# Optimization experiments

Measured on AMD Instinct MI355X. Metric: run time of the kernel, lower is better.

The kernel has to match this reference:

```python
import jax, jax.numpy as jnp
from jax import lax
import numpy as np

NEG = -10000.0

def sequence_mask(length, max_len):
    # [B, max_len] bool
    return jnp.arange(max_len)[None, :] < length[:, None]

def mdn_loss(logp, text_lengths, mel_lengths):
    # logp: [B, T_seq, T_mel]; CTC-style forward recursion over T_mel
    B, T_seq, T_mel = logp.shape
    init = jnp.full((B, T_seq), NEG, logp.dtype).at[:, 0].set(logp[:, 0, 0])
    logp_t = jnp.moveaxis(logp, 2, 0)  # [T_mel, B, T_seq]

    def step(alpha, lp):  # alpha: [B, T_seq]
        shifted = jnp.concatenate(
            [jnp.full((B, 1), NEG, alpha.dtype), alpha[:, :-1]], axis=1)
        new = jnp.logaddexp(alpha + 1e-4, shifted + 1e-4) + lp
        return new, new

    _, cols = lax.scan(step, init, logp_t[1:])
    log_alpha = jnp.concatenate([init[None], cols], axis=0)  # [T_mel, B, T_seq]
    alpha_last = log_alpha[mel_lengths - 1, jnp.arange(B), text_lengths - 1]
    return -alpha_last.mean() / T_seq

def mse_loss_masked(x, target, length):
    # seq_len_norm=False branch: sum of masked squared error / mask.sum() over expanded mask
    B, T, D = x.shape
    mask = sequence_mask(length, T)[:, :, None].astype(x.dtype)  # [B, T, 1]
    diff = x * mask - target * mask
    return jnp.sum(diff * diff) / (jnp.sum(mask) * D)

def sample_wise_min_max(x, mask):
    # x: [B, T, D], mask: [B, T, 1] bool; min/max over dims (1,2)
    maximum = jnp.max(jnp.where(mask, x, 0.0), axis=(1, 2), keepdims=True)
    minimum = jnp.min(jnp.where(mask, x, jnp.inf), axis=(1, 2), keepdims=True)
    return (x - minimum) / (maximum - minimum + 1e-8)

def _gaussian_kernel(size=11, sigma=1.5):
    coords = jnp.arange(size, dtype=jnp.float32) - (size - 1) / 2.0
    g = jnp.exp(-(coords ** 2) / (2.0 * sigma ** 2))
    g = g / g.sum()
    return jnp.outer(g, g)

def _ssim_mean(x, y):
    # x, y: [B, 1, H, W]; 11x11 gaussian SSIM, VALID conv, k1=0.01, k2=0.03, data_range=1
    k = _gaussian_kernel()[None, None].astype(x.dtype)  # [1,1,11,11]
    conv = lambda z: lax.conv_general_dilated(z, k, (1, 1), 'VALID')
    mu_x, mu_y = conv(x), conv(y)
    sxx = conv(x * x) - mu_x * mu_x
    syy = conv(y * y) - mu_y * mu_y
    sxy = conv(x * y) - mu_x * mu_y
    c1, c2 = 0.01 ** 2, 0.03 ** 2
    cs = (2.0 * sxy + c2) / (sxx + syy + c2)
    ssim_map = ((2.0 * mu_x * mu_y + c1) / (mu_x * mu_x + mu_y * mu_y + c1)) * cs
    return ssim_map.mean()

def ssim_loss(y_hat, y, length):
    mask = sequence_mask(length, y.shape[1])[:, :, None]  # [B, T, 1] bool
    y_norm = sample_wise_min_max(y, mask)
    y_hat_norm = sample_wise_min_max(y_hat, mask)
    m = mask.astype(y.dtype)
    loss = 1.0 - _ssim_mean((y_norm * m)[:, None], (y_hat_norm * m)[:, None])
    return jnp.clip(loss, 0.0, 1.0)

SSIM_ALPHA = 1.0
DUR_ALPHA = 1.0
SPEC_ALPHA = 1.0
MDN_ALPHA = 1.0

def setup_inputs() -> dict:
    key = jax.random.key(0)
    ks = jax.random.split(key, 8)
    B, T_seq, T_mel, D = 64, 256, 2048, 80
    logp = jax.random.normal(ks[0], (B, T_seq, T_mel), jnp.float32)
    decoder_output = jax.random.normal(ks[1], (B, T_mel, D), jnp.float32)
    decoder_target = jax.random.uniform(ks[2], (B, T_mel, D), jnp.float32)
    dur_output = jax.random.normal(ks[3], (B, T_seq), jnp.float32)
    dur_target = jax.random.uniform(ks[4], (B, T_seq), jnp.float32)
    decoder_output_lens = jax.random.randint(ks[5], (B,), T_mel // 2, T_mel + 1)
    input_lens = jax.random.randint(ks[6], (B,), T_seq // 2, T_seq + 1)
    return {
        'logp': logp,
        'decoder_output': decoder_output,
        'decoder_target': decoder_target,
        'dur_output': dur_output,
        'dur_target': dur_target,
        'decoder_output_lens': decoder_output_lens,
        'input_lens': input_lens,
        'phase': 4,
    }

def reference(logp, decoder_output, decoder_target, dur_output, dur_target,
              decoder_output_lens, input_lens, phase):
    spec_l = ssim_l = dur_l = mdn_l = 0.0
    if phase == 0:
        mdn_l = mdn_loss(logp, input_lens, decoder_output_lens)
    elif phase == 1:
        spec_l = mse_loss_masked(decoder_output, decoder_target, decoder_output_lens)
        ssim_l = ssim_loss(decoder_output, decoder_target, decoder_output_lens)
    elif phase == 2:
        mdn_l = mdn_loss(logp, input_lens, decoder_output_lens)
        spec_l = mse_loss_masked(decoder_output, decoder_target, decoder_output_lens)
        ssim_l = ssim_loss(decoder_output, decoder_target, decoder_output_lens)
    elif phase == 3:
        dur_l = mse_loss_masked(dur_output[:, :, None], dur_target[:, :, None], input_lens)
    else:
        mdn_l = mdn_loss(logp, input_lens, decoder_output_lens)
        spec_l = mse_loss_masked(decoder_output, decoder_target, decoder_output_lens)
        ssim_l = ssim_loss(decoder_output, decoder_target, decoder_output_lens)
        dur_l = mse_loss_masked(dur_output[:, :, None], dur_target[:, :, None], input_lens)
    loss = SPEC_ALPHA * spec_l + SSIM_ALPHA * ssim_l + DUR_ALPHA * dur_l + MDN_ALPHA * mdn_l
    return loss
```

## Files before the change

### kernel.cpp

```cpp
#include <hip/hip_runtime.h>
#include <math.h>

typedef unsigned short u16;
typedef unsigned int u32;

#define INV_LN2 1.44269504088896f
#define LN2     0.693147180559945f
#define NEG2    (-14426.9504f)
#define SEG1T   18


struct Ws {
  double ssim_sum;
  double dur_sum;
  double spec_part[256];
  float  mnT[256], mxT[256], mnO[256], mxO[256];
  float  A[64 * 256];
  float  Bv[64 * 256];
  float  ckF[64 * 256];
  float  ckB[64 * 256];
};

__device__ __forceinline__ float lse2f(float a, float b) {
  float m = fmaxf(a, b);
  float d = fabsf(a - b);
  return m + __builtin_amdgcn_logf(1.0f + __builtin_amdgcn_exp2f(-d));
}
__device__ __forceinline__ float lae2g(float a, float b, float g) {
  float m = fmaxf(a, b);
  float d = fabsf(a - b);
  return (m + g) + __builtin_amdgcn_logf(1.0f + __builtin_amdgcn_exp2f(-d));
}
__device__ __forceinline__ u16 bf16rn(float f) {
  u32 u = __float_as_uint(f);
  u32 r = (u + 0x7fffu + ((u >> 16) & 1u)) >> 16;
  return (u16)r;
}

constexpr float G11[11] = {
  0.00102838f, 0.00759876f, 0.03600077f, 0.10936070f, 0.21300554f,
  0.26601172f,
  0.21300554f, 0.10936070f, 0.03600077f, 0.00759876f, 0.00102838f};

#define TSTR 264
#define TSZ  (32 * TSTR)

__device__ __forceinline__ void stage_tile(const float* __restrict__ gb, int kb,
                                           u16* dst, int tid) {
  const int ltid = tid - 64;
  const int tb = kb << 5;
#pragma unroll
  for (int it = 0; it < 11; ++it) {
    int i = ltid + it * 192;
    if (i < 2048) {
      int s = i >> 3, e = i & 7;
      float4 v = *(const float4*)(gb + (size_t)s * 2048 + tb + 4 * e);
      u16* d = dst + (4 * e) * TSTR + s;
      d[0]        = bf16rn(v.x * INV_LN2);
      d[TSTR]     = bf16rn(v.y * INV_LN2);
      d[2 * TSTR] = bf16rn(v.z * INV_LN2);
      d[3 * TSTR] = bf16rn(v.w * INV_LN2);
    }
  }
}

__global__ __launch_bounds__(256) void kseg1(
    const float* __restrict__ logp,
    const float* __restrict__ deco, const float* __restrict__ dect,
    const float* __restrict__ duro, const float* __restrict__ durt,
    const int* __restrict__ mel_lens, const int* __restrict__ inp_lens,
    Ws* __restrict__ ws) {
  __shared__ u16 TB[2 * TSZ];
  __shared__ float L[5][4];
  const int bid = blockIdx.x, tid = threadIdx.x;
  const int l = tid;

  if (bid < 64) {
    const int b = bid;
    const float* gb = logp + (size_t)b * 256 * 2048;
    if (tid < 64) __builtin_amdgcn_s_setprio(2);
    else __builtin_amdgcn_s_setprio(1);
    float a0 = NEG2, a1 = NEG2, a2 = NEG2, a3 = NEG2;
    if (tid < 64 && l == 0) a0 = gb[0] * INV_LN2;
    auto FWD = [&](uint2 fg) {
      float g0 = __uint_as_float(fg.x << 16);
      float g1 = __uint_as_float(fg.x & 0xffff0000u);
      float g2 = __uint_as_float(fg.y << 16);
      float g3 = __uint_as_float(fg.y & 0xffff0000u);
      int up = __builtin_amdgcn_update_dpp(
          __float_as_int(NEG2), __float_as_int(a3), 0x138, 0xF, 0xF, false);
      float am1 = __int_as_float(up);
      float n0 = lae2g(a0, am1, g0);
      float n1 = lae2g(a1, a0, g1);
      float n2 = lae2g(a2, a1, g2);
      float n3 = lae2g(a3, a2, g3);
      a0 = n0; a1 = n1; a2 = n2; a3 = n3;
    };
    if (tid >= 64) stage_tile(gb, 0, TB, tid);
    __syncthreads();
    if (tid >= 64) stage_tile(gb, 1, TB + TSZ, tid);
    else {
      const u16* fs = TB + 4 * l;
      for (int i = 1; i < 32; ++i) FWD(*(const uint2*)(fs + i * TSTR));
    }
    __syncthreads();
    for (int j = 1; j < SEG1T; ++j) {
      if (tid >= 64) {
        if (j < SEG1T - 1) stage_tile(gb, j + 1, TB + ((j + 1) & 1) * TSZ, tid);
      } else {
        const u16* fs = TB + (j & 1) * TSZ + 4 * l;
        uint2 fb[2][4];
#pragma unroll
        for (int k = 0; k < 4; ++k) fb[0][k] = *(const uint2*)(fs + k * TSTR);
#pragma unroll
        for (int g = 0; g < 8; ++g) {
          const int cur = g & 1, nxt = cur ^ 1;
          if (g < 7) {
#pragma unroll
            for (int k = 0; k < 4; ++k)
              fb[nxt][k] = *(const uint2*)(fs + ((g + 1) * 4 + k) * TSTR);
          }
#pragma unroll
          for (int k = 0; k < 4; ++k) FWD(fb[cur][k]);
        }
      }
      __syncthreads();
    }
    if (tid < 64)
      *(float4*)&ws->ckF[b * 256 + 4 * l] = make_float4(a0, a1, a2, a3);
    return;
  }

  if (bid < 128) {
    const int b = bid - 64;
    const int T = mel_lens[b] - 1;
    const int ss = inp_lens[b] - 1;
    const int kbT = T >> 5;
    const float* gb = logp + (size_t)b * 256 * 2048;
    if (tid < 64) __builtin_amdgcn_s_setprio(2);
    else __builtin_amdgcn_s_setprio(1);
    float b0 = NEG2, b1 = NEG2, b2 = NEG2, b3 = NEG2;
    if (tid < 64) {
      b0 = (4 * l + 0 == ss) ? 0.f : NEG2;
      b1 = (4 * l + 1 == ss) ? 0.f : NEG2;
      b2 = (4 * l + 2 == ss) ? 0.f : NEG2;
      b3 = (4 * l + 3 == ss) ? 0.f : NEG2;
    }
    auto BWD = [&](uint2 bg, bool act) {
      float g0 = __uint_as_float(bg.x << 16);
      float g1 = __uint_as_float(bg.x & 0xffff0000u);
      float g2 = __uint_as_float(bg.y << 16);
      float g3 = __uint_as_float(bg.y & 0xffff0000u);
      float c0 = b0 + g0, c1 = b1 + g1, c2 = b2 + g2, c3 = b3 + g3;
      int dn = __builtin_amdgcn_update_dpp(
          __float_as_int(NEG2), __float_as_int(c0), 0x130, 0xF, 0xF, false);
      float cp = __int_as_float(dn);
      float m0 = lse2f(c0, c1);
      float m1 = lse2f(c1, c2);
      float m2 = lse2f(c2, c3);
      float m3 = lse2f(c3, cp);
      b0 = act ? m0 : b0; b1 = act ? m1 : b1;
      b2 = act ? m2 : b2; b3 = act ? m3 : b3;
    };
    if (tid >= 64) { if (kbT >= 32) stage_tile(gb, kbT, TB, tid); }
    __syncthreads();
    if (tid >= 64) {
      if (kbT - 1 >= 32) stage_tile(gb, kbT - 1, TB + TSZ, tid);
    } else if (kbT >= 32) {
      const u16* bs = TB + 4 * l;
      for (int ii = 31; ii >= 0; --ii) {
        int tt = (kbT << 5) + ii;
        if (tt <= T) BWD(*(const uint2*)(bs + ii * TSTR), true);
      }
    }
    __syncthreads();
    for (int j = 1; j < SEG1T; ++j) {
      if (tid >= 64) {
        int bk = kbT - j - 1;
        if (j < SEG1T - 1 && bk >= 32) stage_tile(gb, bk, TB + ((j + 1) & 1) * TSZ, tid);
      } else {
        const u16* bs = TB + (j & 1) * TSZ + 4 * l;
        const bool act = (kbT - j) >= 32;
        uint2 bb[2][4];
#pragma unroll
        for (int k = 0; k < 4; ++k) bb[0][k] = *(const uint2*)(bs + (31 - k) * TSTR);
#pragma unroll
        for (int g = 0; g < 8; ++g) {
          const int cur = g & 1, nxt = cur ^ 1;
          if (g < 7) {
#pragma unroll
            for (int k = 0; k < 4; ++k)
              bb[nxt][k] = *(const uint2*)(bs + (31 - ((g + 1) * 4 + k)) * TSTR);
          }
#pragma unroll
          for (int k = 0; k < 4; ++k) BWD(bb[cur][k], act);
        }
      }
      __syncthreads();
    }
    if (tid < 64)
      *(float4*)&ws->ckB[b * 256 + 4 * l] = make_float4(b0, b1, b2, b3);
    return;
  }

  if (bid < 384) {
    int idx = bid - 128, b = idx >> 2, part = idx & 3;
    int len = mel_lens[b];
    int rbeg = part * 512;
    int rcnt = len - rbeg; rcnt = rcnt < 0 ? 0 : (rcnt > 512 ? 512 : rcnt);
    float mnT = __builtin_inff(), mxT = -__builtin_inff();
    float mnO = __builtin_inff(), mxO = -__builtin_inff();
    float ssum = 0.f;
    if (rcnt > 0) {
      const float4* po = (const float4*)(deco + ((size_t)(b * 2048 + rbeg)) * 80);
      const float4* pt = (const float4*)(dect + ((size_t)(b * 2048 + rbeg)) * 80);
      int n4 = rcnt * 20;
      for (int i = tid; i < n4; i += 256) {
        float4 vo = po[i], vt = pt[i];
        mnO = fminf(mnO, fminf(fminf(vo.x, vo.y), fminf(vo.z, vo.w)));
        mxO = fmaxf(mxO, fmaxf(fmaxf(vo.x, vo.y), fmaxf(vo.z, vo.w)));
        mnT = fminf(mnT, fminf(fminf(vt.x, vt.y), fminf(vt.z, vt.w)));
        mxT = fmaxf(mxT, fmaxf(fmaxf(vt.x, vt.y), fmaxf(vt.z, vt.w)));
        float dx = vo.x - vt.x, dy = vo.y - vt.y, dz = vo.z - vt.z, dw = vo.w - vt.w;
        ssum += dx * dx + dy * dy + dz * dz + dw * dw;
      }
    }
    for (int o = 32; o; o >>= 1) {
      mnT = fminf(mnT, __shfl_xor(mnT, o));
      mxT = fmaxf(mxT, __shfl_xor(mxT, o));
      mnO = fminf(mnO, __shfl_xor(mnO, o));
      mxO = fmaxf(mxO, __shfl_xor(mxO, o));
      ssum += __shfl_xor(ssum, o);
    }
    int w = tid >> 6;
    if ((tid & 63) == 0) { L[0][w] = mnT; L[1][w] = mxT; L[2][w] = mnO; L[3][w] = mxO; L[4][w] = ssum; }
    __syncthreads();
    if (tid == 0) {
      mnT = fminf(fminf(L[0][0], L[0][1]), fminf(L[0][2], L[0][3]));
      mxT = fmaxf(fmaxf(L[1][0], L[1][1]), fmaxf(L[1][2], L[1][3]));
      mnO = fminf(fminf(L[2][0], L[2][1]), fminf(L[2][2], L[2][3]));
      mxO = fmaxf(fmaxf(L[3][0], L[3][1]), fmaxf(L[3][2], L[3][3]));
      ssum = L[4][0] + L[4][1] + L[4][2] + L[4][3];
      ws->mnT[idx] = mnT; ws->mxT[idx] = mxT; ws->mnO[idx] = mnO; ws->mxO[idx] = mxO;
      ws->spec_part[idx] = (double)ssum;
    }
    return;
  }

  {
    float ssum = 0.f;
    for (int i = tid; i < 64 * 256; i += 256) {
      int b2 = i >> 8, s2 = i & 255;
      if (s2 < inp_lens[b2]) { float d = duro[i] - durt[i]; ssum += d * d; }
    }
    for (int o = 32; o; o >>= 1) ssum += __shfl_xor(ssum, o);
    int w = tid >> 6;
    if ((tid & 63) == 0) L[4][w] = ssum;
    __syncthreads();
    if (tid == 0) {
      ws->dur_sum = (double)(L[4][0] + L[4][1] + L[4][2] + L[4][3]);
      ws->ssim_sum = 0.0;
    }
  }
}

__global__ __launch_bounds__(256) void kseg2(
    const float* __restrict__ logp,
    const float* __restrict__ deco, const float* __restrict__ dect,
    const int* __restrict__ mel_lens, const int* __restrict__ inp_lens,
    Ws* __restrict__ ws) {
  __shared__ float SMF[14704];
  const int bid = blockIdx.x, tid = threadIdx.x;
  const int l = tid;
  u16* TB = (u16*)SMF;

  if (bid < 64) {
    const int b = bid;
    const float* gb = logp + (size_t)b * 256 * 2048;
    if (tid < 64) __builtin_amdgcn_s_setprio(2);
    else __builtin_amdgcn_s_setprio(1);
    float a0 = NEG2, a1 = NEG2, a2 = NEG2, a3 = NEG2;
    if (tid < 64) {
      float4 c = *(const float4*)&ws->ckF[b * 256 + 4 * l];
      a0 = c.x; a1 = c.y; a2 = c.z; a3 = c.w;
    }
    auto FWD = [&](uint2 fg) {
      float g0 = __uint_as_float(fg.x << 16);
      float g1 = __uint_as_float(fg.x & 0xffff0000u);
      float g2 = __uint_as_float(fg.y << 16);
      float g3 = __uint_as_float(fg.y & 0xffff0000u);
      int up = __builtin_amdgcn_update_dpp(
          __float_as_int(NEG2), __float_as_int(a3), 0x138, 0xF, 0xF, false);
      float am1 = __int_as_float(up);
      float n0 = lae2g(a0, am1, g0);
      float n1 = lae2g(a1, a0, g1);
      float n2 = lae2g(a2, a1, g2);
      float n3 = lae2g(a3, a2, g3);
      a0 = n0; a1 = n1; a2 = n2; a3 = n3;
    };
    if (tid >= 64) stage_tile(gb, SEG1T, TB, tid);
    __syncthreads();
    for (int j = SEG1T; j < 32; ++j) {
      if (tid >= 64) {
        if (j < 31) stage_tile(gb, j + 1, TB + ((j + 1) & 1) * TSZ, tid);
      } else {
        const u16* fs = TB + (j & 1) * TSZ + 4 * l;
        uint2 fb[2][4];
#pragma unroll
        for (int k = 0; k < 4; ++k) fb[0][k] = *(const uint2*)(fs + k * TSTR);
#pragma unroll
        for (int g = 0; g < 8; ++g) {
          const int cur = g & 1, nxt = cur ^ 1;
          if (g < 7) {
#pragma unroll
            for (int k = 0; k < 4; ++k)
              fb[nxt][k] = *(const uint2*)(fs + ((g + 1) * 4 + k) * TSTR);
          }
#pragma unroll
          for (int k = 0; k < 4; ++k) FWD(fb[cur][k]);
        }
      }
      __syncthreads();
    }
    if (tid < 64)
      *(float4*)&ws->A[b * 256 + 4 * l] = make_float4(a0, a1, a2, a3);
    return;
  }

  if (bid < 128) {
    const int b = bid - 64;
    const int T = mel_lens[b] - 1;
    const int kbT = T >> 5;
    float b0 = NEG2, b1 = NEG2, b2 = NEG2, b3 = NEG2;
    if (tid < 64) {
      float4 c = *(const float4*)&ws->ckB[b * 256 + 4 * l];
      b0 = c.x; b1 = c.y; b2 = c.z; b3 = c.w;
    }
    if (kbT - SEG1T < 32) {
      if (tid < 64)
        *(float4*)&ws->Bv[b * 256 + 4 * l] = make_float4(b0, b1, b2, b3);
      return;
    }
    const float* gb = logp + (size_t)b * 256 * 2048;
    if (tid < 64) __builtin_amdgcn_s_setprio(2);
    else __builtin_amdgcn_s_setprio(1);
    auto BWD = [&](uint2 bg, bool act) {
      float g0 = __uint_as_float(bg.x << 16);
      float g1 = __uint_as_float(bg.x & 0xffff0000u);
      float g2 = __uint_as_float(bg.y << 16);
      float g3 = __uint_as_float(bg.y & 0xffff0000u);
      float c0 = b0 + g0, c1 = b1 + g1, c2 = b2 + g2, c3 = b3 + g3;
      int dn = __builtin_amdgcn_update_dpp(
          __float_as_int(NEG2), __float_as_int(c0), 0x130, 0xF, 0xF, false);
      float cp = __int_as_float(dn);
      float m0 = lse2f(c0, c1);
      float m1 = lse2f(c1, c2);
      float m2 = lse2f(c2, c3);
      float m3 = lse2f(c3, cp);
      b0 = act ? m0 : b0; b1 = act ? m1 : b1;
      b2 = act ? m2 : b2; b3 = act ? m3 : b3;
    };
    if (tid >= 64) stage_tile(gb, kbT - SEG1T, TB, tid);
    __syncthreads();
    for (int j = SEG1T; j < 32; ++j) {
      if (tid >= 64) {
        int bk = kbT - j - 1;
        if (j < 31 && bk >= 32) stage_tile(gb, bk, TB + ((j + 1) & 1) * TSZ, tid);
      } else {
        const u16* bs = TB + (j & 1) * TSZ + 4 * l;
        const bool act = (kbT - j) >= 32;
        uint2 bb[2][4];
#pragma unroll
        for (int k = 0; k < 4; ++k) bb[0][k] = *(const uint2*)(bs + (31 - k) * TSTR);
#pragma unroll
        for (int g = 0; g < 8; ++g) {
          const int cur = g & 1, nxt = cur ^ 1;
          if (g < 7) {
#pragma unroll
            for (int k = 0; k < 4; ++k)
              bb[nxt][k] = *(const uint2*)(bs + (31 - ((g + 1) * 4 + k)) * TSTR);
          }
#pragma unroll
          for (int k = 0; k < 4; ++k) BWD(bb[cur][k], act);
        }
      }
      __syncthreads();
    }
    if (tid < 64)
      *(float4*)&ws->Bv[b * 256 + 4 * l] = make_float4(b0, b1, b2, b3);
    return;
  }

  float* cc = SMF;
  float* R = SMF + 14700;
  int cix = bid - 128;
  int b = cix >> 6, tile = cix & 63;
  int r0 = tile * 32;
  int nrows = 2038 - r0; nrows = nrows > 32 ? 32 : nrows;
  int nin = nrows + 10;
  int len = mel_lens[b];
  float mnT = fminf(fminf(ws->mnT[4 * b], ws->mnT[4 * b + 1]), fminf(ws->mnT[4 * b + 2], ws->mnT[4 * b + 3]));
  float mxT = fmaxf(fmaxf(ws->mxT[4 * b], ws->mxT[4 * b + 1]), fmaxf(ws->mxT[4 * b + 2], ws->mxT[4 * b + 3]));
  float mnO = fminf(fminf(ws->mnO[4 * b], ws->mnO[4 * b + 1]), fminf(ws->mnO[4 * b + 2], ws->mnO[4 * b + 3]));
  float mxO = fmaxf(fmaxf(ws->mxO[4 * b], ws->mxO[4 * b + 1]), fmaxf(ws->mxO[4 * b + 2], ws->mxO[4 * b + 3]));
  if (len < 2048) { mxT = fmaxf(mxT, 0.f); mxO = fmaxf(mxO, 0.f); }
  float sT = 1.0f / (mxT - mnT + 1e-8f);
  float sO = 1.0f / (mxO - mnO + 1e-8f);
  const float* po = deco + (size_t)b * 2048 * 80;
  const float* pt = dect + (size_t)b * 2048 * 80;

  for (int p = tid; p < nin * 70; p += 256) {
    int r = p / 70, j = p - 70 * r;
    int grow = r0 + r;
    float s0 = 0, s1 = 0, s2 = 0, s3 = 0, s4 = 0;
    if (grow < len) {
      const float* ro = po + (size_t)grow * 80 + j;
      const float* rt = pt + (size_t)grow * 80 + j;
#pragma unroll
      for (int k = 0; k < 11; ++k) {
        float tn = (rt[k] - mnT) * sT;
        float on = (ro[k] - mnO) * sO;
        float g = G11[k];
        s0 = fmaf(g, tn, s0);
        s1 = fmaf(g, on, s1);
        s2 = fmaf(g * tn, tn, s2);
        s3 = fmaf(g * on, on, s3);
        s4 = fmaf(g * tn, on, s4);
      }
    }
    cc[p] = s0; cc[2940 + p] = s1; cc[2 * 2940 + p] = s2;
    cc[3 * 2940 + p] = s3; cc[4 * 2940 + p] = s4;
  }
  __syncthreads();

  float acc = 0.f;
  for (int q = tid; q < nrows * 70; q += 256) {
    int i = q / 70, j = q - 70 * i;
    float mx = 0, my = 0, xx = 0, yy = 0, xy = 0;
#pragma unroll
    for (int k = 0; k < 11; ++k) {
      float g = G11[k];
      int o = (i + k) * 70 + j;
      mx = fmaf(g, cc[o], mx);
      my = fmaf(g, cc[2940 + o], my);
      xx = fmaf(g, cc[2 * 2940 + o], xx);
      yy = fmaf(g, cc[3 * 2940 + o], yy);
      xy = fmaf(g, cc[4 * 2940 + o], xy);
    }
    float vx = xx - mx * mx, vy = yy - my * my, vxy = xy - mx * my;
    float cs = (2.f * vxy + 9e-4f) / (vx + vy + 9e-4f);
    float lum = (2.f * mx * my + 1e-4f) / (mx * mx + my * my + 1e-4f);
    acc += lum * cs;
  }
  for (int o = 32; o; o >>= 1) acc += __shfl_xor(acc, o);
  if ((tid & 63) == 0) R[tid >> 6] = acc;
  __syncthreads();
  if (tid == 0) atomicAdd(&ws->ssim_sum, (double)(R[0] + R[1] + R[2] + R[3]));
}

__global__ __launch_bounds__(256) void kfin(
    const int* __restrict__ mel_lens, const int* __restrict__ inp_lens,
    Ws* __restrict__ ws, float* __restrict__ out) {
  __shared__ float MD[64];
  __shared__ double LD[4][4];
  int tid = threadIdx.x;
  {
    int b = tid >> 2, q = tid & 3;
    const float* Ab = ws->A + b * 256;
    const float* Bb = ws->Bv + b * 256;
    float mx = -3.0e38f;
    for (int j = q; j < 256; j += 4) mx = fmaxf(mx, Ab[j] + Bb[j]);
    mx = fmaxf(mx, __shfl_xor(mx, 1));
    mx = fmaxf(mx, __shfl_xor(mx, 2));
    float se = 0.f;
    for (int j = q; j < 256; j += 4)
      se += __builtin_amdgcn_exp2f(Ab[j] + Bb[j] - mx);
    se += __shfl_xor(se, 1);
    se += __shfl_xor(se, 2);
    if (q == 0)
      MD[b] = LN2 * (mx + __builtin_amdgcn_logf(se)) + (float)(mel_lens[b] - 1) * 1e-4f;
  }
  __syncthreads();
  double sp = ws->spec_part[tid];
  double md = 0.0, ml = 0.0, il = 0.0;
  if (tid < 64) {
    md = (double)MD[tid];
    ml = (double)mel_lens[tid];
    il = (double)inp_lens[tid];
  }
  for (int o = 32; o; o >>= 1) {
    sp += __shfl_xor(sp, o);
    md += __shfl_xor(md, o);
    ml += __shfl_xor(ml, o);
    il += __shfl_xor(il, o);
  }
  int w = tid >> 6;
  if ((tid & 63) == 0) { LD[w][0] = sp; LD[w][1] = md; LD[w][2] = ml; LD[w][3] = il; }
  __syncthreads();
  if (tid == 0) {
    sp = LD[0][0] + LD[1][0] + LD[2][0] + LD[3][0];
    md = LD[0][1] + LD[1][1] + LD[2][1] + LD[3][1];
    ml = LD[0][2] + LD[1][2] + LD[2][2] + LD[3][2];
    il = LD[0][3] + LD[1][3] + LD[2][3] + LD[3][3];
    double spec = sp / (ml * 80.0);
    double dur = ws->dur_sum / il;
    double mdn = -(md / 64.0) / 256.0;
    double sm = ws->ssim_sum / (64.0 * 2038.0 * 70.0);
    double sl = 1.0 - sm;
    sl = sl < 0.0 ? 0.0 : (sl > 1.0 ? 1.0 : sl);
    out[0] = (float)(spec + sl + dur + mdn);
  }
}

extern "C" void kernel_launch(void* const* d_in, const int* in_sizes, int n_in,
                              void* d_out, int out_size, void* d_ws, size_t ws_size,
                              hipStream_t stream) {
  const float* logp = (const float*)d_in[0];
  const float* deco = (const float*)d_in[1];
  const float* dect = (const float*)d_in[2];
  const float* duro = (const float*)d_in[3];
  const float* durt = (const float*)d_in[4];
  const int* mel_lens = (const int*)d_in[5];
  const int* inp_lens = (const int*)d_in[6];
  Ws* ws = (Ws*)d_ws;
  hipLaunchKernelGGL(kseg1, dim3(385), dim3(256), 0, stream,
                     logp, deco, dect, duro, durt, mel_lens, inp_lens, ws);
  hipLaunchKernelGGL(kseg2, dim3(128 + 64 * 64), dim3(256), 0, stream,
                     logp, deco, dect, mel_lens, inp_lens, ws);
  hipLaunchKernelGGL(kfin, dim3(1), dim3(256), 0, stream,
                     mel_lens, inp_lens, ws, (float*)d_out);
}
```

Before: 187.1 us.

## Stage normalized SSIM input rows in LDS and split columns into two halves

The SSIM blocks of kseg2 now load each input row segment once into shared memory, normalized, instead of re-reading 11 overlapping global values per output column. The 70 output columns are processed in two halves of 35, which shrinks the intermediate horizontal-conv buffers and lowers the kernel's shared memory size. That smaller LDS footprint may let more blocks fit per CU, which also matters for the recursion blocks that share the same allocation. The cost is extra __syncthreads per half and some recomputed overlap columns between the halves.

```diff
diff --git a/kernel.cpp b/kernel.cpp
--- a/kernel.cpp
+++ b/kernel.cpp
@@ -44,6 +44,9 @@
 
 #define TSTR 264
 #define TSZ  (32 * TSTR)
+
+#define CC_CH (42 * 36)
+#define SMFN2 11432
 
 __device__ __forceinline__ void stage_tile(const float* __restrict__ gb, int kb,
                                            u16* dst, int tid) {
@@ -269,7 +272,7 @@
     const float* __restrict__ deco, const float* __restrict__ dect,
     const int* __restrict__ mel_lens, const int* __restrict__ inp_lens,
     Ws* __restrict__ ws) {
-  __shared__ float SMF[14704];
+  __shared__ float SMF[SMFN2];
   const int bid = blockIdx.x, tid = threadIdx.x;
   const int l = tid;
   u16* TB = (u16*)SMF;
@@ -391,8 +394,10 @@
     return;
   }
 
-  float* cc = SMF;
-  float* R = SMF + 14700;
+  float* RWt = SMF;
+  float* RWo = SMF + 1932;
+  float* cc  = SMF + 3864;
+  float* R   = SMF + 3864 + 5 * CC_CH;
   int cix = bid - 128;
   int b = cix >> 6, tile = cix & 63;
   int r0 = tile * 32;
@@ -409,48 +414,64 @@
   const float* po = deco + (size_t)b * 2048 * 80;
   const float* pt = dect + (size_t)b * 2048 * 80;
 
-  for (int p = tid; p < nin * 70; p += 256) {
-    int r = p / 70, j = p - 70 * r;
-    int grow = r0 + r;
-    float s0 = 0, s1 = 0, s2 = 0, s3 = 0, s4 = 0;
-    if (grow < len) {
-      const float* ro = po + (size_t)grow * 80 + j;
-      const float* rt = pt + (size_t)grow * 80 + j;
+  float acc = 0.f;
+#pragma unroll
+  for (int h = 0; h < 2; ++h) {
+    const int jb = h * 35;
+    for (int idx = tid; idx < nin * 45; idx += 256) {
+      int r = idx / 45, c = idx - 45 * r;
+      int grow = r0 + r;
+      float vt = 0.f, vo = 0.f;
+      if (grow < len) {
+        float a = pt[(size_t)grow * 80 + jb + c];
+        float o = po[(size_t)grow * 80 + jb + c];
+        vt = (a - mnT) * sT;
+        vo = (o - mnO) * sO;
+      }
+      RWt[r * 46 + c] = vt;
+      RWo[r * 46 + c] = vo;
+    }
+    __syncthreads();
+
+    for (int p = tid; p < nin * 35; p += 256) {
+      int r = p / 35, jj = p - 35 * r;
+      const float* rt = RWt + r * 46 + jj;
+      const float* ro = RWo + r * 46 + jj;
+      float s0 = 0, s1 = 0, s2 = 0, s3 = 0, s4 = 0;
 #pragma unroll
       for (int k = 0; k < 11; ++k) {
-        float tn = (rt[k] - mnT) * sT;
-        float on = (ro[k] - mnO) * sO;
-        float g = G11[k];
+        float tn = rt[k], on = ro[k], g = G11[k];
         s0 = fmaf(g, tn, s0);
         s1 = fmaf(g, on, s1);
         s2 = fmaf(g * tn, tn, s2);
         s3 = fmaf(g * on, on, s3);
         s4 = fmaf(g * tn, on, s4);
       }
-    }
-    cc[p] = s0; cc[2940 + p] = s1; cc[2 * 2940 + p] = s2;
-    cc[3 * 2940 + p] = s3; cc[4 * 2940 + p] = s4;
-  }
-  __syncthreads();
-
-  float acc = 0.f;
-  for (int q = tid; q < nrows * 70; q += 256) {
-    int i = q / 70, j = q - 70 * i;
-    float mx = 0, my = 0, xx = 0, yy = 0, xy = 0;
-#pragma unroll
-    for (int k = 0; k < 11; ++k) {
-      float g = G11[k];
-      int o = (i + k) * 70 + j;
-      mx = fmaf(g, cc[o], mx);
-      my = fmaf(g, cc[2940 + o], my);
-      xx = fmaf(g, cc[2 * 2940 + o], xx);
-      yy = fmaf(g, cc[3 * 2940 + o], yy);
-      xy = fmaf(g, cc[4 * 2940 + o], xy);
-    }
-    float vx = xx - mx * mx, vy = yy - my * my, vxy = xy - mx * my;
-    float cs = (2.f * vxy + 9e-4f) / (vx + vy + 9e-4f);
-    float lum = (2.f * mx * my + 1e-4f) / (mx * mx + my * my + 1e-4f);
-    acc += lum * cs;
+      int o = r * 36 + jj;
+      cc[o] = s0; cc[CC_CH + o] = s1; cc[2 * CC_CH + o] = s2;
+      cc[3 * CC_CH + o] = s3; cc[4 * CC_CH + o] = s4;
+    }
+    __syncthreads();
+
+    for (int q = tid; q < nrows * 35; q += 256) {
+      int i = q / 35, jj = q - 35 * i;
+      float mx = 0, my = 0, xx = 0, yy = 0, xy = 0;
+#pragma unroll
+      for (int k = 0; k < 11; ++k) {
+        float g = G11[k];
+        int o = (i + k) * 36 + jj;
+        mx = fmaf(g, cc[o], mx);
+        my = fmaf(g, cc[CC_CH + o], my);
+        xx = fmaf(g, cc[2 * CC_CH + o], xx);
+        yy = fmaf(g, cc[3 * CC_CH + o], yy);
+        xy = fmaf(g, cc[4 * CC_CH + o], xy);
+      }
+      float vx = xx - mx * mx, vy = yy - my * my, vxy = xy - mx * my;
+      float cs = (2.f * vxy + 9e-4f) / (vx + vy + 9e-4f);
+      float lum = (2.f * mx * my + 1e-4f) / (mx * mx + my * my + 1e-4f);
+      acc += lum * cs;
+    }
+    __syncthreads();
   }
   for (int o = 32; o; o >>= 1) acc += __shfl_xor(acc, o);
   if ((tid & 63) == 0) R[tid >> 6] = acc;
```

New measurement: 202.5 us. 8.3% more time.
